# Kernel optimization log

Hardware: AMD Instinct MI355X
Metric: run time of the kernel (lower is better)

The kernel has to match this reference:

```python
import jax, jax.numpy as jnp
import numpy as np

B, C, H, W = 8, 256, 64, 64
CQK = C // 8  # 32


def setup_inputs() -> dict:
    key = jax.random.key(0)
    ks = jax.random.split(key, 7)
    s = 0.02
    return {
        "feat_map": jax.random.normal(ks[0], (B, C, H, W), dtype=jnp.float32),
        "w1": jax.random.normal(ks[1], (CQK, C), dtype=jnp.float32) * s,
        "b1": jnp.zeros((CQK,), dtype=jnp.float32),
        "w2": jax.random.normal(ks[2], (CQK, C), dtype=jnp.float32) * s,
        "b2": jnp.zeros((CQK,), dtype=jnp.float32),
        "w3": jax.random.normal(ks[3], (C, C), dtype=jnp.float32) * s,
        "b3": jnp.zeros((C,), dtype=jnp.float32),
        "gamma": jnp.zeros((1,), dtype=jnp.float32),
    }


def reference(feat_map, w1, b1, w2, b2, w3, b3, gamma):
    b, c, h, w = feat_map.shape
    n = h * w
    x = feat_map.reshape(b, c, n)  # [B, C, N]
    # 1x1 convs == per-pixel linear maps over channels
    q = jnp.einsum("oc,bcn->bno", w1, x) + b1  # [B, N, C//8]
    k = jnp.einsum("oc,bcn->bon", w2, x) + b2[None, :, None]  # [B, C//8, N]
    v = jnp.einsum("oc,bcn->bon", w3, x) + b3[None, :, None]  # [B, C, N]
    relation = jnp.einsum("bno,bom->bnm", q, k)  # [B, N, N]
    attn = jax.nn.softmax(relation, axis=-1)  # softmax over last dim
    # feat_refine = bmm(v, attn^T): out[:, :, i] = sum_j v[:, :, j] * attn[i, j]
    feat_refine = jnp.einsum("bcm,bnm->bcn", v, attn).reshape(b, c, h, w)
    scaled = gamma[0] * feat_refine
    return (feat_refine, scaled)
```

## Files before the change

### kernel.cpp

```cpp
#include <hip/hip_runtime.h>
#include <cmath>

#define NB 8
#define CC 256
#define NPIX 4096
#define QB 128
#define KVB 64
#define NT2 32
#define LOG2E 1.4426950408889634f

typedef __attribute__((ext_vector_type(4))) float f32x4;
typedef __attribute__((ext_vector_type(16))) float f32x16;
typedef __attribute__((ext_vector_type(8))) short s16x8;
typedef __attribute__((ext_vector_type(4))) unsigned int u32x4;
typedef __attribute__((ext_vector_type(2))) unsigned int u32x2;

__device__ __forceinline__ unsigned short f2bf(float f) {
    union { float f; unsigned int u; } v; v.f = f;
    return (unsigned short)((v.u + 0x7FFFu + ((v.u >> 16) & 1u)) >> 16);
}

__device__ __forceinline__ unsigned int cvt_pk_bf16(float lo, float hi) {
    unsigned int r;
    asm("v_cvt_pk_bf16_f32 %0, %1, %2" : "=v"(r) : "v"(lo), "v"(hi));
    return r;
}

__device__ __forceinline__ float u2f(unsigned int u) {
    union { unsigned int u; float f; } v; v.u = u; return v.f;
}

__global__ __launch_bounds__(320) void proj_gemm_kernel(
    const float* __restrict__ x,
    const float* __restrict__ w1, const float* __restrict__ b1,
    const float* __restrict__ w2, const float* __restrict__ b2,
    const float* __restrict__ w3, const float* __restrict__ b3,
    unsigned short* __restrict__ Qm, unsigned short* __restrict__ Km,
    unsigned short* __restrict__ Vm)
{
    const int b  = blockIdx.x >> 6;
    const int n0 = (blockIdx.x & 63) * 64;
    const int wave = threadIdx.x >> 6;
    const int lane = threadIdx.x & 63;
    const int cl = lane & 15, g = lane >> 4;

    const float* arow[4];
#pragma unroll
    for (int ct = 0; ct < 4; ++ct) {
        const int row = wave * 64 + ct * 16 + cl;
        if (row < 32)       arow[ct] = w1 + (size_t)row * 256;
        else if (row < 64)  arow[ct] = w2 + (size_t)(row - 32) * 256;
        else                arow[ct] = w3 + (size_t)(row - 64) * 256;
    }

    const float* xb = x + (size_t)b * CC * NPIX + n0 + cl;

    f32x4 acc[4][4];
#pragma unroll
    for (int ct = 0; ct < 4; ++ct)
#pragma unroll
        for (int nt = 0; nt < 4; ++nt) acc[ct][nt] = (f32x4){0.f, 0.f, 0.f, 0.f};

    for (int ks = 0; ks < 8; ++ks) {
        const int c0 = ks * 32;
        s16x8 ah[4];
#pragma unroll
        for (int ct = 0; ct < 4; ++ct) {
            const float* ap = arow[ct] + c0 + g * 8;
            f32x4 a0 = *(const f32x4*)ap;
            f32x4 a1 = *(const f32x4*)(ap + 4);
            u32x4 u;
            u[0] = cvt_pk_bf16(a0[0], a0[1]); u[1] = cvt_pk_bf16(a0[2], a0[3]);
            u[2] = cvt_pk_bf16(a1[0], a1[1]); u[3] = cvt_pk_bf16(a1[2], a1[3]);
            ah[ct] = __builtin_bit_cast(s16x8, u);
        }
#pragma unroll
        for (int nt = 0; nt < 4; ++nt) {
            const float* xp = xb + (size_t)(c0 + g * 8) * NPIX + nt * 16;
            float xe[8];
#pragma unroll
            for (int e = 0; e < 8; ++e) xe[e] = xp[(size_t)e * NPIX];
            u32x4 uh, ul;
#pragma unroll
            for (int p = 0; p < 4; ++p) {
                const unsigned int hp = cvt_pk_bf16(xe[2 * p], xe[2 * p + 1]);
                const float h0 = u2f(hp << 16);
                const float h1 = u2f(hp & 0xffff0000u);
                uh[p] = hp;
                ul[p] = cvt_pk_bf16(xe[2 * p] - h0, xe[2 * p + 1] - h1);
            }
            const s16x8 bh = __builtin_bit_cast(s16x8, uh);
            const s16x8 bl = __builtin_bit_cast(s16x8, ul);
#pragma unroll
            for (int ct = 0; ct < 4; ++ct)
                acc[ct][nt] = __builtin_amdgcn_mfma_f32_16x16x32_bf16(ah[ct], bh, acc[ct][nt], 0, 0, 0);
#pragma unroll
            for (int ct = 0; ct < 4; ++ct)
                acc[ct][nt] = __builtin_amdgcn_mfma_f32_16x16x32_bf16(ah[ct], bl, acc[ct][nt], 0, 0, 0);
        }
    }

    if (wave == 0) {
#pragma unroll
        for (int ct = 0; ct < 4; ++ct) {
#pragma unroll
            for (int nt = 0; nt < 4; ++nt) {
                const int n = n0 + nt * 16 + cl;
                const int co = ct * 16 + g * 4;
                f32x4 v = acc[ct][nt];
                if (ct < 2) {
                    const float q0 = (v[0] + b1[co + 0]) * LOG2E;
                    const float q1 = (v[1] + b1[co + 1]) * LOG2E;
                    const float q2 = (v[2] + b1[co + 2]) * LOG2E;
                    const float q3 = (v[3] + b1[co + 3]) * LOG2E;
                    u32x2 dd = {cvt_pk_bf16(q0, q1), cvt_pk_bf16(q2, q3)};
                    *(u32x2*)(Qm + ((size_t)b * NPIX + n) * 32 + co) = dd;
                } else {
                    const int ko = co - 32;
                    const float k0 = v[0] + b2[ko + 0];
                    const float k1 = v[1] + b2[ko + 1];
                    const float k2 = v[2] + b2[ko + 2];
                    const float k3 = v[3] + b2[ko + 3];
                    u32x2 dd = {cvt_pk_bf16(k0, k1), cvt_pk_bf16(k2, k3)};
                    *(u32x2*)(Km + ((size_t)b * NPIX + n) * 32 + ko) = dd;
                }
            }
        }
    } else {
        const int cvb = (wave - 1) * 64;
#pragma unroll
        for (int ct = 0; ct < 4; ++ct) {
#pragma unroll
            for (int nt = 0; nt < 4; ++nt) {
                const int n = n0 + nt * 16 + cl;
                const int cv = cvb + ct * 16 + g * 4;
#pragma unroll
                for (int r = 0; r < 4; ++r)
                    Vm[((size_t)b * CC + cv + r) * NPIX + n] = f2bf(acc[ct][nt][r] + b3[cv + r]);
            }
        }
    }
}

__global__ __launch_bounds__(512, 2) void attn_kernel(
    const unsigned short* __restrict__ Qm, const unsigned short* __restrict__ Km,
    const unsigned short* __restrict__ Vm, const float* __restrict__ gamma,
    float* __restrict__ out)
{
    __shared__ unsigned short Vs[2][2][CC * KVB];
    __shared__ float mArr[2][4][32];
    __shared__ float lArr[2][4][32];

    const int bid = ((blockIdx.x & 7) << 5) + (blockIdx.x >> 3);
    const int b = bid >> 5;
    const int q0 = (bid & 31) * QB;

    const int t = threadIdx.x;
    const int wave = t >> 6;
    const int lane = t & 63;
    const int q_ = lane & 31;
    const int hi = lane >> 5;
    const int s = wave & 3;
    const int h = wave >> 2;

    const int qrow = q0 + s * 32 + q_;

    s16x8 qf[2];
#pragma unroll
    for (int kh = 0; kh < 2; ++kh)
        qf[kh] = *(const s16x8*)(Qm + ((size_t)b * NPIX + qrow) * 32 + kh * 16 + hi * 8);

    f32x16 acc[8];
#pragma unroll
    for (int ct = 0; ct < 8; ++ct) acc[ct] = (f32x16){};

    float mrun = -__builtin_inff();
    float lrun = 0.f;

    const unsigned short* Kg = Km + (size_t)b * NPIX * 32;
    const unsigned short* Vg = Vm + (size_t)b * CC * NPIX;

    const int tg = t & 255;
    const int vr0 = tg >> 3;
    const int cg = (tg & 7) ^ (vr0 & 7);
    const unsigned short* vsrc = Vg + (size_t)vr0 * NPIX + cg * 8;

#define STAGE_V(tile, buf_)                                                    \
    {                                                                          \
        const int mm_ = h * 2048 + (tile) * KVB;                               \
        _Pragma("unroll")                                                      \
        for (int i_ = 0; i_ < 8; ++i_)                                         \
            __builtin_amdgcn_global_load_lds(                                  \
                (const __attribute__((address_space(1))) void*)(vsrc + (size_t)i_ * 32 * NPIX + mm_), \
                (__attribute__((address_space(3))) void*)(&Vs[h][buf_][i_ * 2048 + tg * 8]), \
                16, 0, 0);                                                     \
    }

    s16x8 kf[2][2];
#define LOAD_KF(mm_)                                                           \
    {                                                                          \
        _Pragma("unroll")                                                      \
        for (int mt_ = 0; mt_ < 2; ++mt_)                                      \
            _Pragma("unroll")                                                  \
            for (int kh_ = 0; kh_ < 2; ++kh_)                                  \
                kf[mt_][kh_] = *(const s16x8*)(Kg + (size_t)((mm_) + 32 * mt_ + q_) * 32 + kh_ * 16 + hi * 8); \
    }

    STAGE_V(0, 0)
    LOAD_KF(h * 2048)

    int cur = 0;
    for (int it = 0; it < NT2; ++it) {
        __syncthreads();

        if (it < NT2 - 1) STAGE_V(it + 1, cur ^ 1)

        f32x16 z = (f32x16){};
        f32x16 s0 = __builtin_amdgcn_mfma_f32_32x32x16_bf16(kf[0][0], qf[0], z, 0, 0, 0);
        s0 = __builtin_amdgcn_mfma_f32_32x32x16_bf16(kf[0][1], qf[1], s0, 0, 0, 0);
        f32x16 s1 = __builtin_amdgcn_mfma_f32_32x32x16_bf16(kf[1][0], qf[0], z, 0, 0, 0);
        s1 = __builtin_amdgcn_mfma_f32_32x32x16_bf16(kf[1][1], qf[1], s1, 0, 0, 0);

        LOAD_KF(h * 2048 + (((it + 1) & (NT2 - 1))) * KVB)

        float ml = -__builtin_inff();
#pragma unroll
        for (int r = 0; r < 16; ++r) ml = fmaxf(ml, s0[r]);
#pragma unroll
        for (int r = 0; r < 16; ++r) ml = fmaxf(ml, s1[r]);

        if (!__all(ml <= mrun + 8.f)) {
            ml = fmaxf(ml, __shfl_xor(ml, 32, 64));
            const float mnew = fmaxf(mrun, ml);
            const float alpha = __builtin_amdgcn_exp2f(mrun - mnew);
            mrun = mnew;
            lrun *= alpha;
#pragma unroll
            for (int ct = 0; ct < 8; ++ct) acc[ct] *= alpha;
        }

#pragma unroll
        for (int r = 0; r < 16; ++r) { s0[r] = __builtin_amdgcn_exp2f(s0[r] - mrun); lrun += s0[r]; }
#pragma unroll
        for (int r = 0; r < 16; ++r) { s1[r] = __builtin_amdgcn_exp2f(s1[r] - mrun); lrun += s1[r]; }

        unsigned int w0[4][2], w1[4][2];
#pragma unroll
        for (int p = 0; p < 4; ++p) {
            w0[p][0] = cvt_pk_bf16(s0[4 * p + 0], s0[4 * p + 1]);
            w0[p][1] = cvt_pk_bf16(s0[4 * p + 2], s0[4 * p + 3]);
            w1[p][0] = cvt_pk_bf16(s1[4 * p + 0], s1[4 * p + 1]);
            w1[p][1] = cvt_pk_bf16(s1[4 * p + 2], s1[4 * p + 3]);
        }

#pragma unroll
        for (int t4 = 0; t4 < 4; ++t4) {
            const int lt = t4 & 1;
            unsigned int a0 = (t4 < 2) ? w0[2 * lt][0] : w1[2 * lt][0];
            unsigned int b0 = (t4 < 2) ? w0[2 * lt + 1][0] : w1[2 * lt + 1][0];
            unsigned int a1 = (t4 < 2) ? w0[2 * lt][1] : w1[2 * lt][1];
            unsigned int b1 = (t4 < 2) ? w0[2 * lt + 1][1] : w1[2 * lt + 1][1];
            asm("v_permlane32_swap_b32 %0, %1" : "+v"(a0), "+v"(b0));
            asm("v_permlane32_swap_b32 %0, %1" : "+v"(a1), "+v"(b1));
            u32x4 bw = {a0, a1, b0, b1};
            const s16x8 pb = __builtin_bit_cast(s16x8, bw);

            __builtin_amdgcn_s_setprio(1);
#pragma unroll
            for (int ct = 0; ct < 8; ++ct) {
                const int c = 32 * ct + q_;
                const int slot = (2 * t4 + hi) ^ (c & 7);
                const s16x8 av = *(const s16x8*)(&Vs[h][cur][c * 64 + slot * 8]);
                acc[ct] = __builtin_amdgcn_mfma_f32_32x32x16_bf16(av, pb, acc[ct], 0, 0, 0);
            }
            __builtin_amdgcn_s_setprio(0);
        }

        cur ^= 1;
    }

    lrun += __shfl_xor(lrun, 32, 64);

    __syncthreads();

    if (lane < 32) { mArr[h][s][lane] = mrun; lArr[h][s][lane] = lrun; }
    __syncthreads();

    const float m_o = mArr[h ^ 1][s][q_];
    const float l_o = lArr[h ^ 1][s][q_];
    const float M = fmaxf(mrun, m_o);
    const float f = __builtin_amdgcn_exp2f(mrun - M);
    const float l_tot = lrun * f + l_o * __builtin_amdgcn_exp2f(m_o - M);

    float* S = (float*)&Vs[0][0][0];
    if (h == 1) {
#pragma unroll
        for (int ct = 0; ct < 8; ++ct)
#pragma unroll
            for (int r = 0; r < 16; ++r)
                S[(ct * 16 + r) * 256 + s * 64 + lane] = acc[ct][r] * f;
    }
    __syncthreads();

    if (h == 0) {
        const float inv = 1.f / l_tot;
        const float gm = gamma[0];
        float* out2 = out + (size_t)NB * CC * NPIX;
        const int n = qrow;
#pragma unroll
        for (int ct = 0; ct < 8; ++ct) {
#pragma unroll
            for (int r = 0; r < 16; ++r) {
                const int c = 32 * ct + (r & 3) + 8 * (r >> 2) + 4 * hi;
                const float val = (acc[ct][r] * f + S[(ct * 16 + r) * 256 + s * 64 + lane]) * inv;
                const size_t idx = ((size_t)b * CC + c) * NPIX + n;
                out[idx] = val;
                out2[idx] = gm * val;
            }
        }
    }
}

extern "C" void kernel_launch(void* const* d_in, const int* in_sizes, int n_in,
                              void* d_out, int out_size, void* d_ws, size_t ws_size,
                              hipStream_t stream) {
    (void)in_sizes; (void)n_in; (void)out_size; (void)ws_size;
    const float* x     = (const float*)d_in[0];
    const float* w1    = (const float*)d_in[1];
    const float* b1    = (const float*)d_in[2];
    const float* w2    = (const float*)d_in[3];
    const float* b2    = (const float*)d_in[4];
    const float* w3    = (const float*)d_in[5];
    const float* b3    = (const float*)d_in[6];
    const float* gamma = (const float*)d_in[7];
    float* out = (float*)d_out;

    unsigned short* Qm = (unsigned short*)d_ws;
    unsigned short* Km = Qm + (size_t)NB * NPIX * 32;
    unsigned short* Vm = Km + (size_t)NB * NPIX * 32;

    proj_gemm_kernel<<<NB * 64, 320, 0, stream>>>(x, w1, b1, w2, b2, w3, b3, Qm, Km, Vm);
    attn_kernel<<<NB * 32, 512, 0, stream>>>(Qm, Km, Vm, gamma, out);
}
```

Before: 124.6 us.

## Stagger wave halves so one runs PV MFMAs while the other computes softmax

Splits the per-tile loop into QK, softmax/pack, and PV stages. Waves in half h==1 run a software-pipelined order: they issue the previous tile's PV MFMAs before the current QK and softmax, offsetting them from the h==0 waves so matrix-core and VALU/transcendental work interleave across waves. The max and sum reductions also become trees instead of serial chains. The cost is more live registers for the packed P fragments, a different prefetch schedule for h==1 (same-iteration staging), and an extra PV tail after the loop.

```diff
diff --git a/kernel.cpp b/kernel.cpp
--- a/kernel.cpp
+++ b/kernel.cpp
@@ -206,82 +206,118 @@
                 kf[mt_][kh_] = *(const s16x8*)(Kg + (size_t)((mm_) + 32 * mt_ + q_) * 32 + kh_ * 16 + hi * 8); \
     }
 
-    STAGE_V(0, 0)
-    LOAD_KF(h * 2048)
+#define QK_TILE()                                                              \
+    {                                                                          \
+        f32x16 z_ = (f32x16){};                                                \
+        s0 = __builtin_amdgcn_mfma_f32_32x32x16_bf16(kf[0][0], qf[0], z_, 0, 0, 0); \
+        s0 = __builtin_amdgcn_mfma_f32_32x32x16_bf16(kf[0][1], qf[1], s0, 0, 0, 0); \
+        s1 = __builtin_amdgcn_mfma_f32_32x32x16_bf16(kf[1][0], qf[0], z_, 0, 0, 0); \
+        s1 = __builtin_amdgcn_mfma_f32_32x32x16_bf16(kf[1][1], qf[1], s1, 0, 0, 0); \
+    }
+
+#define SOFTMAX_PACK(PW_)                                                      \
+    {                                                                          \
+        float tm_[16];                                                         \
+        _Pragma("unroll")                                                      \
+        for (int i_ = 0; i_ < 16; ++i_) tm_[i_] = fmaxf(s0[i_], s1[i_]);       \
+        _Pragma("unroll")                                                      \
+        for (int i_ = 0; i_ < 8; ++i_) tm_[i_] = fmaxf(tm_[i_], tm_[i_ + 8]);  \
+        _Pragma("unroll")                                                      \
+        for (int i_ = 0; i_ < 4; ++i_) tm_[i_] = fmaxf(tm_[i_], tm_[i_ + 4]);  \
+        const float ml_ = fmaxf(fmaxf(tm_[0], tm_[1]), fmaxf(tm_[2], tm_[3])); \
+        if (!__all(ml_ <= mrun + 8.f)) {                                       \
+            float mw_ = fmaxf(ml_, __shfl_xor(ml_, 32, 64));                   \
+            const float mnew_ = fmaxf(mrun, mw_);                              \
+            const float alpha_ = __builtin_amdgcn_exp2f(mrun - mnew_);         \
+            mrun = mnew_;                                                      \
+            lrun *= alpha_;                                                    \
+            _Pragma("unroll")                                                  \
+            for (int ct_ = 0; ct_ < 8; ++ct_) acc[ct_] *= alpha_;              \
+        }                                                                      \
+        _Pragma("unroll")                                                      \
+        for (int r_ = 0; r_ < 16; ++r_) {                                      \
+            s0[r_] = __builtin_amdgcn_exp2f(s0[r_] - mrun);                    \
+            s1[r_] = __builtin_amdgcn_exp2f(s1[r_] - mrun);                    \
+        }                                                                      \
+        float ts_[16];                                                         \
+        _Pragma("unroll")                                                      \
+        for (int i_ = 0; i_ < 16; ++i_) ts_[i_] = s0[i_] + s1[i_];             \
+        _Pragma("unroll")                                                      \
+        for (int i_ = 0; i_ < 8; ++i_) ts_[i_] += ts_[i_ + 8];                 \
+        _Pragma("unroll")                                                      \
+        for (int i_ = 0; i_ < 4; ++i_) ts_[i_] += ts_[i_ + 4];                 \
+        lrun += (ts_[0] + ts_[1]) + (ts_[2] + ts_[3]);                         \
+        unsigned int w0_[4][2], w1_[4][2];                                     \
+        _Pragma("unroll")                                                      \
+        for (int p_ = 0; p_ < 4; ++p_) {                                       \
+            w0_[p_][0] = cvt_pk_bf16(s0[4 * p_ + 0], s0[4 * p_ + 1]);          \
+            w0_[p_][1] = cvt_pk_bf16(s0[4 * p_ + 2], s0[4 * p_ + 3]);          \
+            w1_[p_][0] = cvt_pk_bf16(s1[4 * p_ + 0], s1[4 * p_ + 1]);          \
+            w1_[p_][1] = cvt_pk_bf16(s1[4 * p_ + 2], s1[4 * p_ + 3]);          \
+        }                                                                      \
+        _Pragma("unroll")                                                      \
+        for (int t4_ = 0; t4_ < 4; ++t4_) {                                    \
+            const int lt_ = t4_ & 1;                                           \
+            unsigned int a0_ = (t4_ < 2) ? w0_[2 * lt_][0] : w1_[2 * lt_][0];  \
+            unsigned int b0_ = (t4_ < 2) ? w0_[2 * lt_ + 1][0] : w1_[2 * lt_ + 1][0]; \
+            unsigned int a1_ = (t4_ < 2) ? w0_[2 * lt_][1] : w1_[2 * lt_][1];  \
+            unsigned int b1_ = (t4_ < 2) ? w0_[2 * lt_ + 1][1] : w1_[2 * lt_ + 1][1]; \
+            asm("v_permlane32_swap_b32 %0, %1" : "+v"(a0_), "+v"(b0_));        \
+            asm("v_permlane32_swap_b32 %0, %1" : "+v"(a1_), "+v"(b1_));        \
+            PW_[t4_] = (u32x4){a0_, a1_, b0_, b1_};                            \
+        }                                                                      \
+    }
+
+#define PV_TILE(bufsel_, PW_)                                                  \
+    {                                                                          \
+        __builtin_amdgcn_s_setprio(1);                                         \
+        _Pragma("unroll")                                                      \
+        for (int t4_ = 0; t4_ < 4; ++t4_) {                                    \
+            const s16x8 pb_ = __builtin_bit_cast(s16x8, PW_[t4_]);             \
+            _Pragma("unroll")                                                  \
+            for (int ct_ = 0; ct_ < 8; ++ct_) {                                \
+                const int c_ = 32 * ct_ + q_;                                  \
+                const int slot_ = (2 * t4_ + hi) ^ (c_ & 7);                   \
+                const s16x8 av_ = *(const s16x8*)(&Vs[h][bufsel_][c_ * 64 + slot_ * 8]); \
+                acc[ct_] = __builtin_amdgcn_mfma_f32_32x32x16_bf16(av_, pb_, acc[ct_], 0, 0, 0); \
+            }                                                                  \
+        }                                                                      \
+        __builtin_amdgcn_s_setprio(0);                                         \
+    }
+
+    f32x16 s0, s1;
+    u32x4 pw[4];
+    if (h == 0) {
+        STAGE_V(0, 0)
+        LOAD_KF(0)
+    }
 
     int cur = 0;
     for (int it = 0; it < NT2; ++it) {
         __syncthreads();
 
-        if (it < NT2 - 1) STAGE_V(it + 1, cur ^ 1)
-
-        f32x16 z = (f32x16){};
-        f32x16 s0 = __builtin_amdgcn_mfma_f32_32x32x16_bf16(kf[0][0], qf[0], z, 0, 0, 0);
-        s0 = __builtin_amdgcn_mfma_f32_32x32x16_bf16(kf[0][1], qf[1], s0, 0, 0, 0);
-        f32x16 s1 = __builtin_amdgcn_mfma_f32_32x32x16_bf16(kf[1][0], qf[0], z, 0, 0, 0);
-        s1 = __builtin_amdgcn_mfma_f32_32x32x16_bf16(kf[1][1], qf[1], s1, 0, 0, 0);
-
-        LOAD_KF(h * 2048 + (((it + 1) & (NT2 - 1))) * KVB)
-
-        float ml = -__builtin_inff();
-#pragma unroll
-        for (int r = 0; r < 16; ++r) ml = fmaxf(ml, s0[r]);
-#pragma unroll
-        for (int r = 0; r < 16; ++r) ml = fmaxf(ml, s1[r]);
-
-        if (!__all(ml <= mrun + 8.f)) {
-            ml = fmaxf(ml, __shfl_xor(ml, 32, 64));
-            const float mnew = fmaxf(mrun, ml);
-            const float alpha = __builtin_amdgcn_exp2f(mrun - mnew);
-            mrun = mnew;
-            lrun *= alpha;
-#pragma unroll
-            for (int ct = 0; ct < 8; ++ct) acc[ct] *= alpha;
-        }
-
-#pragma unroll
-        for (int r = 0; r < 16; ++r) { s0[r] = __builtin_amdgcn_exp2f(s0[r] - mrun); lrun += s0[r]; }
-#pragma unroll
-        for (int r = 0; r < 16; ++r) { s1[r] = __builtin_amdgcn_exp2f(s1[r] - mrun); lrun += s1[r]; }
-
-        unsigned int w0[4][2], w1[4][2];
-#pragma unroll
-        for (int p = 0; p < 4; ++p) {
-            w0[p][0] = cvt_pk_bf16(s0[4 * p + 0], s0[4 * p + 1]);
-            w0[p][1] = cvt_pk_bf16(s0[4 * p + 2], s0[4 * p + 3]);
-            w1[p][0] = cvt_pk_bf16(s1[4 * p + 0], s1[4 * p + 1]);
-            w1[p][1] = cvt_pk_bf16(s1[4 * p + 2], s1[4 * p + 3]);
-        }
-
-#pragma unroll
-        for (int t4 = 0; t4 < 4; ++t4) {
-            const int lt = t4 & 1;
-            unsigned int a0 = (t4 < 2) ? w0[2 * lt][0] : w1[2 * lt][0];
-            unsigned int b0 = (t4 < 2) ? w0[2 * lt + 1][0] : w1[2 * lt + 1][0];
-            unsigned int a1 = (t4 < 2) ? w0[2 * lt][1] : w1[2 * lt][1];
-            unsigned int b1 = (t4 < 2) ? w0[2 * lt + 1][1] : w1[2 * lt + 1][1];
-            asm("v_permlane32_swap_b32 %0, %1" : "+v"(a0), "+v"(b0));
-            asm("v_permlane32_swap_b32 %0, %1" : "+v"(a1), "+v"(b1));
-            u32x4 bw = {a0, a1, b0, b1};
-            const s16x8 pb = __builtin_bit_cast(s16x8, bw);
-
-            __builtin_amdgcn_s_setprio(1);
-#pragma unroll
-            for (int ct = 0; ct < 8; ++ct) {
-                const int c = 32 * ct + q_;
-                const int slot = (2 * t4 + hi) ^ (c & 7);
-                const s16x8 av = *(const s16x8*)(&Vs[h][cur][c * 64 + slot * 8]);
-                acc[ct] = __builtin_amdgcn_mfma_f32_32x32x16_bf16(av, pb, acc[ct], 0, 0, 0);
-            }
-            __builtin_amdgcn_s_setprio(0);
+        if (h == 0) {
+            if (it < NT2 - 1) STAGE_V(it + 1, cur ^ 1)
+            QK_TILE()
+            LOAD_KF((((it + 1) & (NT2 - 1))) * KVB)
+            SOFTMAX_PACK(pw)
+            PV_TILE(cur, pw)
+        } else {
+            STAGE_V(it, cur)
+            LOAD_KF(2048 + it * KVB)
+            if (it > 0) PV_TILE(cur ^ 1, pw)
+            QK_TILE()
+            SOFTMAX_PACK(pw)
         }
 
         cur ^= 1;
     }
 
+    __syncthreads();
+
+    if (h == 1) PV_TILE((NT2 - 1) & 1, pw)
+
     lrun += __shfl_xor(lrun, 32, 64);
-
-    __syncthreads();
 
     if (lane < 32) { mArr[h][s][lane] = mrun; lArr[h][s][lane] = lrun; }
     __syncthreads();
```

Result: slower. 132.6 us (+6.5%).
